# Performance work log

Hardware: AMD Instinct MI355X
Metric: run time of the kernel (lower is better)

The kernel has to match this reference:

```python
import jax, jax.numpy as jnp
import numpy as np

N, K, M, DIM = 131072, 16, 128, 64


def setup_inputs() -> dict:
    key = jax.random.key(0)
    kx, ks, ka, kb = jax.random.split(key, 4)
    return {
        "x": jax.random.normal(kx, (N, DIM), dtype=jnp.float32),
        "s": jax.random.normal(ks, (K,), dtype=jnp.float32),
        "a": jax.random.normal(ka, (K, M, DIM), dtype=jnp.float32),
        "b": jax.random.normal(kb, (K, M), dtype=jnp.float32),
    }


def reference(x, s, a, b):
    # scores[k, n, m] = x[n, :] @ a[k, m, :] + b[k, m]  (batched GEMM over k)
    scores = jnp.einsum("nd,kmd->knm", x, a) + b[:, None, :]
    # per-expert logsumexp over the m affine pieces -> [k, n]
    lse = jax.nn.logsumexp(scores, axis=-1)
    # signed sum over experts -> [n]
    return jnp.einsum("k,kn->n", s, lse)
```

## Files before the change

### kernel.cpp

```cpp
#include <hip/hip_runtime.h>
#include <hip/hip_bf16.h>

#define NROWS 131072
#define KEXP 16
#define MPC 128
#define DIMD 64

typedef float f32x4  __attribute__((ext_vector_type(4)));
typedef float f32x16 __attribute__((ext_vector_type(16)));
typedef short s16x8  __attribute__((ext_vector_type(8)));

#define L2E 1.4426950408889634f
#define LN2 0.6931471805599453f

static __device__ inline unsigned int b2u(__hip_bfloat162 h) {
    union { __hip_bfloat162 h; unsigned int u; } c;
    c.h = h;
    return c.u;
}

static __device__ inline int4 cvt8s(float4 f0, float4 f1, float sc) {
    __hip_bfloat162 p0 = __float22bfloat162_rn(make_float2(f0.x * sc, f0.y * sc));
    __hip_bfloat162 p1 = __float22bfloat162_rn(make_float2(f0.z * sc, f0.w * sc));
    __hip_bfloat162 p2 = __float22bfloat162_rn(make_float2(f1.x * sc, f1.y * sc));
    __hip_bfloat162 p3 = __float22bfloat162_rn(make_float2(f1.z * sc, f1.w * sc));
    int4 pk;
    pk.x = (int)b2u(p0); pk.y = (int)b2u(p1); pk.z = (int)b2u(p2); pk.w = (int)b2u(p3);
    return pk;
}

static __device__ inline void async_copy16(const void* g, void* l) {
    __builtin_amdgcn_global_load_lds(
        (const __attribute__((address_space(1))) unsigned int*)g,
        (__attribute__((address_space(3))) unsigned int*)l, 16, 0, 0);
}

__global__ void prep_kernel(const float* __restrict__ a, const float* __restrict__ b,
                            short* __restrict__ abff) {
    const int u   = blockIdx.x * 256 + threadIdx.x;
    const int k   = u / 1280;
    const int rem = u - k * 1280;
    const int mt  = rem / 320;
    const int rc  = rem - mt * 320;
    const int c   = rc >> 6;
    const int ul  = rc & 63;
    int4 pk;
    if (c < 4) {
        const float* p = a + (size_t)(k * MPC + mt * 32 + (ul & 31)) * DIMD
                           + c * 16 + (ul >> 5) * 8;
        pk = cvt8s(*(const float4*)(p), *(const float4*)(p + 4), L2E);
    } else {
        pk.x = 0; pk.y = 0; pk.z = 0; pk.w = 0;
        if (ul < 32) {
            union { __hip_bfloat16 h; unsigned short us; } cv;
            cv.h = __float2bfloat16(b[k * MPC + mt * 32 + ul] * L2E);
            pk.x = (int)cv.us;
        }
    }
    *(int4*)(abff + (size_t)u * 8) = pk;
}

__global__ __launch_bounds__(256, 4)
void fused_kernel(const float* __restrict__ x, const float* __restrict__ s,
                  const short* __restrict__ abff, float* __restrict__ out) {
    __shared__ int4 abuf[2][1280];

    const int tid  = threadIdx.x;
    const int w    = tid >> 6;
    const int l    = tid & 63;
    const int ln   = l & 31;
    const int half = l >> 5;

    const int family = blockIdx.x & 1;
    const int r0w    = (blockIdx.x >> 1) * 256 + w * 64;

    union { int4 i; s16x8 v; } Bf[2][4];
#pragma unroll
    for (int nt = 0; nt < 2; ++nt)
#pragma unroll
        for (int c = 0; c < 4; ++c) {
            const float* gp = x + (size_t)(r0w + nt * 32 + ln) * DIMD + c * 16 + half * 8;
            float4 f0 = *(const float4*)(gp);
            float4 f1 = *(const float4*)(gp + 4);
            Bf[nt][c].i = cvt8s(f0, f1, 1.0f);
        }

    union { int4 i; s16x8 v; } Bones;
    Bones.i.x = (half == 0) ? 0x3F80 : 0;
    Bones.i.y = 0; Bones.i.z = 0; Bones.i.w = 0;

    {
        const short* src = abff + (size_t)(family * 8) * 10240;
#pragma unroll
        for (int i = 0; i < 5; ++i) {
            const int ch = w * 5 + i;
            async_copy16(src + ch * 512 + l * 8, (char*)&abuf[0][0] + ch * 1024);
        }
    }
    __syncthreads();

    float racc0 = 0.f, racc1 = 0.f;

    for (int k = 0; k < 8; ++k) {
        const int kf = family * 8 + k;
        const int kb = k & 1;

        if (k + 1 < 8) {
            const short* src = abff + (size_t)(kf + 1) * 10240;
#pragma unroll
            for (int i = 0; i < 5; ++i) {
                const int ch = w * 5 + i;
                async_copy16(src + ch * 512 + l * 8,
                             (char*)&abuf[kb ^ 1][0] + ch * 1024);
            }
        }

        const float sk2 = s[kf] * LN2;
        float esum0 = 0.f, esum1 = 0.f;

#pragma unroll
        for (int mt = 0; mt < 4; ++mt) {
            s16x8 Af[5];
#pragma unroll
            for (int c = 0; c < 5; ++c)
                Af[c] = *(const s16x8*)((const short*)&abuf[kb][0] + (mt * 5 + c) * 512 + l * 8);

            {
                f32x16 acc = {};
#pragma unroll
                for (int c = 0; c < 4; ++c)
                    acc = __builtin_amdgcn_mfma_f32_32x32x16_bf16(Af[c], Bf[0][c].v, acc, 0, 0, 0);
                acc = __builtin_amdgcn_mfma_f32_32x32x16_bf16(Af[4], Bones.v, acc, 0, 0, 0);
                float s0 = 0.f, s1 = 0.f, s2 = 0.f, s3 = 0.f;
#pragma unroll
                for (int r = 0; r < 4; ++r) {
                    s0 += __builtin_amdgcn_exp2f(acc[4 * r + 0]);
                    s1 += __builtin_amdgcn_exp2f(acc[4 * r + 1]);
                    s2 += __builtin_amdgcn_exp2f(acc[4 * r + 2]);
                    s3 += __builtin_amdgcn_exp2f(acc[4 * r + 3]);
                }
                esum0 += (s0 + s1) + (s2 + s3);
            }
            {
                f32x16 acc = {};
#pragma unroll
                for (int c = 0; c < 4; ++c)
                    acc = __builtin_amdgcn_mfma_f32_32x32x16_bf16(Af[c], Bf[1][c].v, acc, 0, 0, 0);
                acc = __builtin_amdgcn_mfma_f32_32x32x16_bf16(Af[4], Bones.v, acc, 0, 0, 0);
                float s0 = 0.f, s1 = 0.f, s2 = 0.f, s3 = 0.f;
#pragma unroll
                for (int r = 0; r < 4; ++r) {
                    s0 += __builtin_amdgcn_exp2f(acc[4 * r + 0]);
                    s1 += __builtin_amdgcn_exp2f(acc[4 * r + 1]);
                    s2 += __builtin_amdgcn_exp2f(acc[4 * r + 2]);
                    s3 += __builtin_amdgcn_exp2f(acc[4 * r + 3]);
                }
                esum1 += (s0 + s1) + (s2 + s3);
            }
        }

        float tot0 = esum0 + __shfl_xor(esum0, 32);
        float tot1 = esum1 + __shfl_xor(esum1, 32);
        racc0 = fmaf(sk2, __log2f(tot0), racc0);
        racc1 = fmaf(sk2, __log2f(tot1), racc1);

        __syncthreads();
    }

    atomicAdd(&out[r0w + half * 32 + ln], half ? racc1 : racc0);
}

extern "C" void kernel_launch(void* const* d_in, const int* in_sizes, int n_in,
                              void* d_out, int out_size, void* d_ws, size_t ws_size,
                              hipStream_t stream) {
    const float* x = (const float*)d_in[0];
    const float* s = (const float*)d_in[1];
    const float* a = (const float*)d_in[2];
    const float* b = (const float*)d_in[3];
    float* out = (float*)d_out;

    short* abff = (short*)d_ws;

    hipMemsetAsync(d_out, 0, (size_t)NROWS * sizeof(float), stream);
    prep_kernel<<<80, 256, 0, stream>>>(a, b, abff);
    fused_kernel<<<NROWS / 128, 256, 0, stream>>>(x, s, abff, out);
}
```

Before: 121.9 us.

## Load expert weights directly from global memory, drop LDS double buffer

Removes the LDS double-buffered async staging of per-expert bf16 weights and the per-iteration block barriers. Each wave now reads its A fragments straight from global memory, relying on L1/L2 caching because the weights are shared by all blocks. It also interleaves the MFMA chains for the two row tiles so they can issue back to back. The risk is higher global load latency with no explicit prefetch, and more register pressure from keeping two accumulators live.

```diff
diff --git a/kernel.cpp b/kernel.cpp
--- a/kernel.cpp
+++ b/kernel.cpp
@@ -29,12 +29,6 @@
     return pk;
 }
 
-static __device__ inline void async_copy16(const void* g, void* l) {
-    __builtin_amdgcn_global_load_lds(
-        (const __attribute__((address_space(1))) unsigned int*)g,
-        (__attribute__((address_space(3))) unsigned int*)l, 16, 0, 0);
-}
-
 __global__ void prep_kernel(const float* __restrict__ a, const float* __restrict__ b,
                             short* __restrict__ abff) {
     const int u   = blockIdx.x * 256 + threadIdx.x;
@@ -63,8 +57,6 @@
 __global__ __launch_bounds__(256, 4)
 void fused_kernel(const float* __restrict__ x, const float* __restrict__ s,
                   const short* __restrict__ abff, float* __restrict__ out) {
-    __shared__ int4 abuf[2][1280];
-
     const int tid  = threadIdx.x;
     const int w    = tid >> 6;
     const int l    = tid & 63;
@@ -89,33 +81,13 @@
     Bones.i.x = (half == 0) ? 0x3F80 : 0;
     Bones.i.y = 0; Bones.i.z = 0; Bones.i.w = 0;
 
-    {
-        const short* src = abff + (size_t)(family * 8) * 10240;
-#pragma unroll
-        for (int i = 0; i < 5; ++i) {
-            const int ch = w * 5 + i;
-            async_copy16(src + ch * 512 + l * 8, (char*)&abuf[0][0] + ch * 1024);
-        }
-    }
-    __syncthreads();
-
     float racc0 = 0.f, racc1 = 0.f;
 
     for (int k = 0; k < 8; ++k) {
-        const int kf = family * 8 + k;
-        const int kb = k & 1;
+        const int   kf   = family * 8 + k;
+        const float sk2  = s[kf] * LN2;
+        const short* base = abff + (size_t)kf * 10240 + l * 8;
 
-        if (k + 1 < 8) {
-            const short* src = abff + (size_t)(kf + 1) * 10240;
-#pragma unroll
-            for (int i = 0; i < 5; ++i) {
-                const int ch = w * 5 + i;
-                async_copy16(src + ch * 512 + l * 8,
-                             (char*)&abuf[kb ^ 1][0] + ch * 1024);
-            }
-        }
-
-        const float sk2 = s[kf] * LN2;
         float esum0 = 0.f, esum1 = 0.f;
 
 #pragma unroll
@@ -123,39 +95,33 @@
             s16x8 Af[5];
 #pragma unroll
             for (int c = 0; c < 5; ++c)
-                Af[c] = *(const s16x8*)((const short*)&abuf[kb][0] + (mt * 5 + c) * 512 + l * 8);
+                Af[c] = *(const s16x8*)(base + (mt * 5 + c) * 512);
+
+            f32x16 accA = {}, accB = {};
+#pragma unroll
+            for (int c = 0; c < 4; ++c) {
+                accA = __builtin_amdgcn_mfma_f32_32x32x16_bf16(Af[c], Bf[0][c].v, accA, 0, 0, 0);
+                accB = __builtin_amdgcn_mfma_f32_32x32x16_bf16(Af[c], Bf[1][c].v, accB, 0, 0, 0);
+            }
+            accA = __builtin_amdgcn_mfma_f32_32x32x16_bf16(Af[4], Bones.v, accA, 0, 0, 0);
+            accB = __builtin_amdgcn_mfma_f32_32x32x16_bf16(Af[4], Bones.v, accB, 0, 0, 0);
 
             {
-                f32x16 acc = {};
-#pragma unroll
-                for (int c = 0; c < 4; ++c)
-                    acc = __builtin_amdgcn_mfma_f32_32x32x16_bf16(Af[c], Bf[0][c].v, acc, 0, 0, 0);
-                acc = __builtin_amdgcn_mfma_f32_32x32x16_bf16(Af[4], Bones.v, acc, 0, 0, 0);
-                float s0 = 0.f, s1 = 0.f, s2 = 0.f, s3 = 0.f;
+                float a0 = 0.f, a1 = 0.f, a2 = 0.f, a3 = 0.f;
+                float b0 = 0.f, b1 = 0.f, b2 = 0.f, b3 = 0.f;
 #pragma unroll
                 for (int r = 0; r < 4; ++r) {
-                    s0 += __builtin_amdgcn_exp2f(acc[4 * r + 0]);
-                    s1 += __builtin_amdgcn_exp2f(acc[4 * r + 1]);
-                    s2 += __builtin_amdgcn_exp2f(acc[4 * r + 2]);
-                    s3 += __builtin_amdgcn_exp2f(acc[4 * r + 3]);
+                    a0 += __builtin_amdgcn_exp2f(accA[4 * r + 0]);
+                    a1 += __builtin_amdgcn_exp2f(accA[4 * r + 1]);
+                    a2 += __builtin_amdgcn_exp2f(accA[4 * r + 2]);
+                    a3 += __builtin_amdgcn_exp2f(accA[4 * r + 3]);
+                    b0 += __builtin_amdgcn_exp2f(accB[4 * r + 0]);
+                    b1 += __builtin_amdgcn_exp2f(accB[4 * r + 1]);
+                    b2 += __builtin_amdgcn_exp2f(accB[4 * r + 2]);
+                    b3 += __builtin_amdgcn_exp2f(accB[4 * r + 3]);
                 }
-                esum0 += (s0 + s1) + (s2 + s3);
-            }
-            {
-                f32x16 acc = {};
-#pragma unroll
-                for (int c = 0; c < 4; ++c)
-                    acc = __builtin_amdgcn_mfma_f32_32x32x16_bf16(Af[c], Bf[1][c].v, acc, 0, 0, 0);
-                acc = __builtin_amdgcn_mfma_f32_32x32x16_bf16(Af[4], Bones.v, acc, 0, 0, 0);
-                float s0 = 0.f, s1 = 0.f, s2 = 0.f, s3 = 0.f;
-#pragma unroll
-                for (int r = 0; r < 4; ++r) {
-                    s0 += __builtin_amdgcn_exp2f(acc[4 * r + 0]);
-                    s1 += __builtin_amdgcn_exp2f(acc[4 * r + 1]);
-                    s2 += __builtin_amdgcn_exp2f(acc[4 * r + 2]);
-                    s3 += __builtin_amdgcn_exp2f(acc[4 * r + 3]);
-                }
-                esum1 += (s0 + s1) + (s2 + s3);
+                esum0 += (a0 + a1) + (a2 + a3);
+                esum1 += (b0 + b1) + (b2 + b3);
             }
         }
 
@@ -163,8 +129,6 @@
         float tot1 = esum1 + __shfl_xor(esum1, 32);
         racc0 = fmaf(sk2, __log2f(tot0), racc0);
         racc1 = fmaf(sk2, __log2f(tot1), racc1);
-
-        __syncthreads();
     }
 
     atomicAdd(&out[r0w + half * 32 + ln], half ? racc1 : racc0);
```

Result: slower. 213.7 us (+75.2%).
